# Kernel optimization log

Hardware: AMD Instinct MI355X
Metric: run time of the kernel (lower is better)

## Reference

```python
import jax, jax.numpy as jnp
import numpy as np

N_NODES = 50000


def gcn_conv(x, W, b, src, dst, n_nodes):
    """PyG GCNConv: h = x @ W; add self-loops; symmetric deg^-1/2 norm; scatter-sum; + bias."""
    h = x @ W  # [N, out]
    # degree including self-loop (edge weight 1)
    ones = jnp.ones(dst.shape[0], dtype=x.dtype)
    deg = jax.ops.segment_sum(ones, dst, num_segments=n_nodes) + 1.0  # [N]
    dinv = jax.lax.rsqrt(deg)  # deg >= 1 always (self-loop)
    # per-edge norm = dinv[src] * dinv[dst]; gather, scale, scatter-add
    msg = h[src] * (dinv[src] * dinv[dst])[:, None]  # [E, out]
    agg = jax.ops.segment_sum(msg, dst, num_segments=n_nodes)
    # self-loop contribution: norm_ii = dinv[i]^2
    agg = agg + h * (dinv * dinv)[:, None]
    return agg + b


def setup_inputs() -> dict:
    key = jax.random.key(0)
    k1, k2, k3, k4, k5 = jax.random.split(key, 5)
    in_dim, hidden_dim = 128, 128
    x = jax.random.normal(k1, (N_NODES, in_dim), dtype=jnp.float32)
    edge_index = jax.random.randint(k2, (2, 800000), 0, N_NODES, dtype=jnp.int64)
    W1 = jax.random.normal(k3, (in_dim, hidden_dim), dtype=jnp.float32) * 0.05
    b1 = jnp.zeros((hidden_dim,), dtype=jnp.float32)
    W2 = jax.random.normal(k4, (hidden_dim, 1), dtype=jnp.float32) * 0.05
    b2 = jnp.zeros((1,), dtype=jnp.float32)
    return {"x": x, "edge_index": edge_index, "W1": W1, "b1": b1, "W2": W2, "b2": b2}


def reference(x, edge_index, W1, b1, W2, b2):
    src, dst = edge_index[0], edge_index[1]
    n = x.shape[0]
    h = gcn_conv(x, W1, b1, src, dst, n)
    h = jax.nn.relu(h)  # dropout is identity in eval mode
    out = gcn_conv(h, W2, b2, src, dst, n)
    return out.squeeze(-1)  # [N]
```

## Files before the change

### kernel.cpp

```cpp
#include <hip/hip_runtime.h>
#include <hip/hip_fp16.h>

#define DIM 128
#define SCAN_TILE 2048
#define NCHK 256
#define BKT_SHIFT 8
#define BCAP 8192

typedef _Float16 half8v __attribute__((ext_vector_type(8)));
typedef float    floatx4 __attribute__((ext_vector_type(4)));

__device__ __forceinline__ void h8_to_f8(float4 raw, float* o) {
    half8v hh = __builtin_bit_cast(half8v, raw);
#pragma unroll
    for (int k = 0; k < 8; ++k) o[k] = (float)hh[k];
}
__device__ __forceinline__ void h8_fma_mix(float4 raw, float dv, float* a) {
    half8v hh = __builtin_bit_cast(half8v, raw);
#pragma unroll
    for (int k = 0; k < 8; ++k) a[k] = fmaf((float)hh[k], dv, a[k]);
}

__global__ __launch_bounds__(256) void init_kernel(const float* __restrict__ W,
                                                   _Float16* __restrict__ Wt,
                                                   int* __restrict__ tile_pub) {
    int i = blockIdx.x * 256 + threadIdx.x;
    if (i < 32) tile_pub[i] = 0;
    if (i < DIM * DIM) {
        int k = i >> 7, c = i & 127;
        Wt[(size_t)c * DIM + k] = (_Float16)W[i];
    }
}

__global__ __launch_bounds__(256) void k1gemm_kernel(const int* __restrict__ dst,
                                                     int E, int n, int nbkt,
                                                     unsigned short* __restrict__ rank_local,
                                                     int* __restrict__ blockhist,
                                                     const float* __restrict__ x,
                                                     const _Float16* __restrict__ Wt,
                                                     __half* __restrict__ hs) {
    const int tid = threadIdx.x;
    const int bid = blockIdx.x;
    const bool isK1 = ((bid & 3) == 0) && ((bid >> 2) < NCHK);
    if (isK1) {
        __shared__ int bhl[256];
        const int cid = bid >> 2;
        const int echk = (E + NCHK - 1) / NCHK;
        const int e0 = cid * echk, e1 = min(E, e0 + echk);
        bhl[tid] = 0;
        __syncthreads();
        for (int e = e0 + tid; e < e1; e += 256) {
            int d = min(max(dst[e], 0), n - 1);
            int r = atomicAdd(&bhl[d >> BKT_SHIFT], 1);
            rank_local[e] = (unsigned short)r;
        }
        __syncthreads();
        for (int b = tid; b < nbkt; b += 256)
            blockhist[b * NCHK + cid] = bhl[b];
        return;
    }
    const int g   = bid - 1 - min(bid >> 2, NCHK - 1);
    const int wv  = tid >> 6;
    const int l   = tid & 63;
    const int lr  = l & 15;
    const int lk  = l >> 4;
    const int brow = g * 64 + wv * 16;
    const int arow = min(brow + lr, n - 1);

    floatx4 acc[8];
#pragma unroll
    for (int ct = 0; ct < 8; ++ct) acc[ct] = (floatx4){0.f, 0.f, 0.f, 0.f};

#pragma unroll
    for (int kb = 0; kb < 4; ++kb) {
        const float* ap = x + (size_t)arow * DIM + kb * 32 + lk * 8;
        float4 a0 = ((const float4*)ap)[0];
        float4 a1 = ((const float4*)ap)[1];
        half8v af;
        af[0] = (_Float16)a0.x; af[1] = (_Float16)a0.y;
        af[2] = (_Float16)a0.z; af[3] = (_Float16)a0.w;
        af[4] = (_Float16)a1.x; af[5] = (_Float16)a1.y;
        af[6] = (_Float16)a1.z; af[7] = (_Float16)a1.w;
#pragma unroll
        for (int ct = 0; ct < 8; ++ct) {
            half8v bf = *(const half8v*)(Wt + (size_t)(ct * 16 + lr) * DIM + kb * 32 + lk * 8);
            acc[ct] = __builtin_amdgcn_mfma_f32_16x16x32_f16(af, bf, acc[ct], 0, 0, 0);
        }
    }
#pragma unroll
    for (int j = 0; j < 4; ++j) {
        int orow = brow + lk * 4 + j;
        if (orow < n) {
#pragma unroll
            for (int ct = 0; ct < 8; ++ct)
                hs[(size_t)orow * DIM + ct * 16 + lr] = __float2half(acc[ct][j]);
        }
    }
}

__global__ __launch_bounds__(256) void scan_kernel(const int* __restrict__ in,
                                                   int L, int* __restrict__ outp,
                                                   int* __restrict__ tile_pub) {
    __shared__ int s[256];
    __shared__ int bbase;
    const int t = threadIdx.x;
    const int b = blockIdx.x;
    const int base = b * SCAN_TILE + t * 8;
    int v[8];
    int tsum = 0;
#pragma unroll
    for (int k = 0; k < 8; ++k) {
        int i = base + k;
        v[k] = (i < L) ? in[i] : 0;
        tsum += v[k];
    }
    s[t] = tsum;
    if (t == 0) bbase = 0;
    __syncthreads();
#pragma unroll
    for (int off = 1; off < 256; off <<= 1) {
        int u = (t >= off) ? s[t - off] : 0;
        __syncthreads();
        s[t] += u;
        __syncthreads();
    }
    if (t == 255)
        __hip_atomic_store(&tile_pub[b], s[255] + 1, __ATOMIC_RELEASE, __HIP_MEMORY_SCOPE_AGENT);
    if (t < b) {
        int val;
        do {
            val = __hip_atomic_load(&tile_pub[t], __ATOMIC_ACQUIRE, __HIP_MEMORY_SCOPE_AGENT);
        } while (val == 0);
        atomicAdd(&bbase, val - 1);
    }
    __syncthreads();
    int run = bbase + s[t] - tsum;
#pragma unroll
    for (int k = 0; k < 8; ++k) {
        int i = base + k;
        if (i < L) outp[i] = run;
        run += v[k];
    }
}

__global__ __launch_bounds__(256) void scat_kernel(const int* __restrict__ src,
                                                   const int* __restrict__ dst,
                                                   const unsigned short* __restrict__ rank_local,
                                                   int E, int n,
                                                   const int* __restrict__ bhoff,
                                                   unsigned int* __restrict__ bedge) {
    const int cid = blockIdx.x;
    const int echk = (E + NCHK - 1) / NCHK;
    const int e0 = cid * echk, e1 = min(E, e0 + echk);
    for (int e = e0 + threadIdx.x; e < e1; e += 256) {
        int s = min(max(src[e], 0), n - 1);
        int d = min(max(dst[e], 0), n - 1);
        int bkt = d >> BKT_SHIFT;
        int pos = bhoff[bkt * NCHK + cid] + rank_local[e];
        bedge[pos] = (unsigned int)s | ((unsigned int)(d & 255) << 16);
    }
}

__global__ __launch_bounds__(256) void bcsr_kernel(const int* __restrict__ bhoff,
                                                   const unsigned int* __restrict__ bedge,
                                                   int E, int n, int nbkt,
                                                   unsigned short* __restrict__ csr,
                                                   int* __restrict__ row_off,
                                                   float* __restrict__ dinv) {
    __shared__ unsigned int ed[BCAP];
    __shared__ unsigned short rk[BCAP];
    __shared__ int h[256], s2[256], offx[256];
    const int t = threadIdx.x;
    const int g = blockIdx.x;
    const int beg = bhoff[g * NCHK];
    const int end = (g == nbkt - 1) ? E : bhoff[(g + 1) * NCHK];
    const int cntb = min(end - beg, BCAP);

    h[t] = 0;
    __syncthreads();
    for (int i = t; i < cntb; i += 256) {
        unsigned int u = bedge[beg + i];
        ed[i] = u;
        rk[i] = (unsigned short)atomicAdd(&h[(u >> 16) & 255], 1);
    }
    __syncthreads();
    int hv = h[t];
    s2[t] = hv;
    __syncthreads();
#pragma unroll
    for (int off = 1; off < 256; off <<= 1) {
        int u = (t >= off) ? s2[t - off] : 0;
        __syncthreads();
        s2[t] += u;
        __syncthreads();
    }
    offx[t] = s2[t] - hv;
    __syncthreads();
    int node = (g << BKT_SHIFT) + t;
    if (node < n) {
        row_off[node] = beg + offx[t];
        dinv[node] = rsqrtf((float)hv + 1.0f);
    }
    if (g == nbkt - 1 && t == 0) row_off[n] = E;
    for (int i = t; i < cntb; i += 256) {
        unsigned int u = ed[i];
        csr[beg + offx[(u >> 16) & 255] + rk[i]] = (unsigned short)(u & 0xFFFF);
    }
}

__global__ __launch_bounds__(256) void gather1_kernel(const int* __restrict__ row_off,
                                                      const unsigned short* __restrict__ csr,
                                                      const __half* __restrict__ hs,
                                                      const float* __restrict__ dinv,
                                                      const float* __restrict__ b1,
                                                      const float* __restrict__ W2,
                                                      float* __restrict__ ss, int n) {
    const int wave = threadIdx.x >> 6;
    const int lane = threadIdx.x & 63;
    const int node = blockIdx.x * 4 + wave;
    if (node >= n) return;

    const int rs = row_off[node];
    const int re = row_off[node + 1];
    const int q = lane & 7;
    const int g = lane >> 3;
    const float4* hs4 = (const float4*)hs;

    float a[16];
#pragma unroll
    for (int k = 0; k < 16; ++k) a[k] = 0.f;

    for (int j = rs + g; j < re; j += 8) {
        int s = csr[j];
        float dvs = dinv[s];
        const float4* rp = hs4 + (size_t)s * 16 + 2 * q;
        float4 r0 = rp[0];
        float4 r1 = rp[1];
        h8_fma_mix(r0, dvs, a);
        h8_fma_mix(r1, dvs, a + 8);
    }

#pragma unroll
    for (int k = 0; k < 16; ++k) {
        a[k] += __shfl_xor(a[k], 8, 64);
        a[k] += __shfl_xor(a[k], 16, 64);
        a[k] += __shfl_xor(a[k], 32, 64);
    }

    float dv = dinv[node];
    float hv[16];
    h8_to_f8(hs4[(size_t)node * 16 + 2 * q], hv);
    h8_to_f8(hs4[(size_t)node * 16 + 2 * q + 1], hv + 8);

    float bv[16], wv[16];
#pragma unroll
    for (int u = 0; u < 4; ++u) {
        float4 bq = ((const float4*)b1)[4 * q + u];
        float4 wq = ((const float4*)W2)[4 * q + u];
        bv[4 * u + 0] = bq.x; bv[4 * u + 1] = bq.y; bv[4 * u + 2] = bq.z; bv[4 * u + 3] = bq.w;
        wv[4 * u + 0] = wq.x; wv[4 * u + 1] = wq.y; wv[4 * u + 2] = wq.z; wv[4 * u + 3] = wq.w;
    }

    float p = 0.f;
#pragma unroll
    for (int k = 0; k < 16; ++k) {
        float h1 = fmaxf(fmaf(dv, fmaf(dv, hv[k], a[k]), bv[k]), 0.f);
        p = fmaf(h1, wv[k], p);
    }
    p += __shfl_xor(p, 1, 64);
    p += __shfl_xor(p, 2, 64);
    p += __shfl_xor(p, 4, 64);
    if (lane == 0) ss[node] = p * dv;
}

__global__ __launch_bounds__(256) void gather2_kernel(const int* __restrict__ row_off,
                                                      const unsigned short* __restrict__ csr,
                                                      const float* __restrict__ ss,
                                                      const float* __restrict__ dinv,
                                                      const float* __restrict__ b2,
                                                      float* __restrict__ out, int n) {
    int i = blockIdx.x * 256 + threadIdx.x;
    if (i >= n) return;
    int rs = row_off[i], re = row_off[i + 1];
    float s0 = 0.f, s1 = 0.f, s2 = 0.f, s3 = 0.f;
    int j = rs;
    for (; j + 3 < re; j += 4) {
        int c0 = csr[j], c1 = csr[j + 1], c2 = csr[j + 2], c3 = csr[j + 3];
        s0 += ss[c0]; s1 += ss[c1]; s2 += ss[c2]; s3 += ss[c3];
    }
    for (; j < re; ++j) s0 += ss[csr[j]];
    out[i] = fmaf(dinv[i], (s0 + s1) + (s2 + s3) + ss[i], b2[0]);
}

extern "C" void kernel_launch(void* const* d_in, const int* in_sizes, int n_in,
                              void* d_out, int out_size, void* d_ws, size_t ws_size,
                              hipStream_t stream) {
    const float* x   = (const float*)d_in[0];
    const int*   ei  = (const int*)d_in[1];
    const float* W1  = (const float*)d_in[2];
    const float* b1  = (const float*)d_in[3];
    const float* W2  = (const float*)d_in[4];
    const float* b2  = (const float*)d_in[5];
    float*       out = (float*)d_out;

    const int n = in_sizes[0] / DIM;
    const int E = in_sizes[1] / 2;
    const int* srcI = ei;
    const int* dstI = ei + E;
    const int nbkt = (n + 255) >> BKT_SHIFT;
    const int L = nbkt * NCHK;
    const int scan_tiles = (L + SCAN_TILE - 1) / SCAN_TILE;

    char* ws = (char*)d_ws;
    size_t off = 0;
    auto alloc = [&](size_t bytes) { void* p = ws + off; off = (off + bytes + 511) & ~(size_t)511; return p; };
    float*          dinv     = (float*)alloc((size_t)n * 4);
    int*            row_off  = (int*)  alloc((size_t)(n + 1) * 4);
    unsigned short* rank_loc = (unsigned short*)alloc((size_t)E * 2);
    int*            bhist    = (int*)  alloc((size_t)L * 4);
    int*            bhoff    = (int*)  alloc((size_t)L * 4);
    int*            tile_pub = (int*)  alloc((size_t)32 * 4);
    unsigned int*   bedge    = (unsigned int*)alloc((size_t)E * 4);
    unsigned short* csr      = (unsigned short*)alloc((size_t)E * 2);
    __half*         hs       = (__half*)alloc((size_t)n * DIM * 2);
    float*          ss       = (float*)alloc((size_t)n * 4);
    _Float16*       Wt       = (_Float16*)alloc((size_t)DIM * DIM * 2);

    const int gemm_blocks = (n + 63) / 64;

    init_kernel<<<64, 256, 0, stream>>>(W1, Wt, tile_pub);
    k1gemm_kernel<<<NCHK + gemm_blocks, 256, 0, stream>>>(dstI, E, n, nbkt, rank_loc,
                                                          bhist, x, Wt, hs);
    scan_kernel<<<scan_tiles, 256, 0, stream>>>(bhist, L, bhoff, tile_pub);
    scat_kernel<<<NCHK, 256, 0, stream>>>(srcI, dstI, rank_loc, E, n, bhoff, bedge);
    bcsr_kernel<<<nbkt, 256, 0, stream>>>(bhoff, bedge, E, n, nbkt, csr, row_off, dinv);
    gather1_kernel<<<(n + 3) / 4, 256, 0, stream>>>(row_off, csr, hs, dinv, b1, W2, ss, n);
    gather2_kernel<<<(n + 255) / 256, 256, 0, stream>>>(row_off, csr, ss, dinv, b2, out, n);
}
```

Measured before the change: 111.7 us.

## Stage CSR neighbor indices and dinv in LDS for 16-node gather1 blocks

gather1 now handles 16 nodes per block, with each wave processing 4 nodes in sequence. Before the gather, the block cooperatively loads the CSR index slice and the matching dinv values into shared memory, up to 512 edges. This takes the dependent csr-then-dinv global load chain out of the inner gather loop and leaves only the hs row loads there. The cost is two block barriers, shared memory use and less parallelism per node, since nodes inside a wave are now processed serially.

```diff
diff --git a/kernel.cpp b/kernel.cpp
--- a/kernel.cpp
+++ b/kernel.cpp
@@ -6,6 +6,8 @@
 #define NCHK 256
 #define BKT_SHIFT 8
 #define BCAP 8192
+#define G1NODES 16
+#define G1CAP 512
 
 typedef _Float16 half8v __attribute__((ext_vector_type(8)));
 typedef float    floatx4 __attribute__((ext_vector_type(4)));
@@ -215,62 +217,94 @@
                                                       const float* __restrict__ b1,
                                                       const float* __restrict__ W2,
                                                       float* __restrict__ ss, int n) {
-    const int wave = threadIdx.x >> 6;
-    const int lane = threadIdx.x & 63;
-    const int node = blockIdx.x * 4 + wave;
-    if (node >= n) return;
-
-    const int rs = row_off[node];
-    const int re = row_off[node + 1];
+    __shared__ unsigned short ecsr[G1CAP];
+    __shared__ float edinv[G1CAP];
+    __shared__ int roff[G1NODES + 1];
+
+    const int tid  = threadIdx.x;
+    const int node0 = blockIdx.x * G1NODES;
+    const int nlast = min(node0 + G1NODES, n);
+
+    if (tid <= G1NODES) {
+        int idx = min(node0 + tid, n);
+        roff[tid] = row_off[idx];
+    }
+    __syncthreads();
+    const int base = roff[0];
+    const int cnt  = roff[nlast - node0] - base;
+    const int staged = min(cnt, G1CAP);
+    for (int i = tid; i < staged; i += 256) {
+        int s = csr[base + i];
+        ecsr[i] = (unsigned short)s;
+        edinv[i] = dinv[s];
+    }
+    __syncthreads();
+
+    const int wave = tid >> 6;
+    const int lane = tid & 63;
     const int q = lane & 7;
     const int g = lane >> 3;
     const float4* hs4 = (const float4*)hs;
 
-    float a[16];
-#pragma unroll
-    for (int k = 0; k < 16; ++k) a[k] = 0.f;
-
-    for (int j = rs + g; j < re; j += 8) {
-        int s = csr[j];
-        float dvs = dinv[s];
-        const float4* rp = hs4 + (size_t)s * 16 + 2 * q;
-        float4 r0 = rp[0];
-        float4 r1 = rp[1];
-        h8_fma_mix(r0, dvs, a);
-        h8_fma_mix(r1, dvs, a + 8);
-    }
-
-#pragma unroll
-    for (int k = 0; k < 16; ++k) {
-        a[k] += __shfl_xor(a[k], 8, 64);
-        a[k] += __shfl_xor(a[k], 16, 64);
-        a[k] += __shfl_xor(a[k], 32, 64);
-    }
-
-    float dv = dinv[node];
-    float hv[16];
-    h8_to_f8(hs4[(size_t)node * 16 + 2 * q], hv);
-    h8_to_f8(hs4[(size_t)node * 16 + 2 * q + 1], hv + 8);
-
-    float bv[16], wv[16];
-#pragma unroll
-    for (int u = 0; u < 4; ++u) {
-        float4 bq = ((const float4*)b1)[4 * q + u];
-        float4 wq = ((const float4*)W2)[4 * q + u];
-        bv[4 * u + 0] = bq.x; bv[4 * u + 1] = bq.y; bv[4 * u + 2] = bq.z; bv[4 * u + 3] = bq.w;
-        wv[4 * u + 0] = wq.x; wv[4 * u + 1] = wq.y; wv[4 * u + 2] = wq.z; wv[4 * u + 3] = wq.w;
-    }
-
-    float p = 0.f;
-#pragma unroll
-    for (int k = 0; k < 16; ++k) {
-        float h1 = fmaxf(fmaf(dv, fmaf(dv, hv[k], a[k]), bv[k]), 0.f);
-        p = fmaf(h1, wv[k], p);
-    }
-    p += __shfl_xor(p, 1, 64);
-    p += __shfl_xor(p, 2, 64);
-    p += __shfl_xor(p, 4, 64);
-    if (lane == 0) ss[node] = p * dv;
+#pragma unroll 1
+    for (int i = 0; i < 4; ++i) {
+        const int node = node0 + wave * 4 + i;
+        if (node >= n) break;
+        const int rsL = roff[wave * 4 + i] - base;
+        const int reL = roff[wave * 4 + i + 1] - base;
+
+        float a[16];
+#pragma unroll
+        for (int k = 0; k < 16; ++k) a[k] = 0.f;
+
+        for (int j = rsL + g; j < reL; j += 8) {
+            int s; float dvs;
+            if (j < G1CAP) {
+                s = ecsr[j];
+                dvs = edinv[j];
+            } else {
+                s = csr[base + j];
+                dvs = dinv[s];
+            }
+            const float4* rp = hs4 + (size_t)s * 16 + 2 * q;
+            float4 r0 = rp[0];
+            float4 r1 = rp[1];
+            h8_fma_mix(r0, dvs, a);
+            h8_fma_mix(r1, dvs, a + 8);
+        }
+
+#pragma unroll
+        for (int k = 0; k < 16; ++k) {
+            a[k] += __shfl_xor(a[k], 8, 64);
+            a[k] += __shfl_xor(a[k], 16, 64);
+            a[k] += __shfl_xor(a[k], 32, 64);
+        }
+
+        float dv = dinv[node];
+        float hv[16];
+        h8_to_f8(hs4[(size_t)node * 16 + 2 * q], hv);
+        h8_to_f8(hs4[(size_t)node * 16 + 2 * q + 1], hv + 8);
+
+        float bv[16], wv[16];
+#pragma unroll
+        for (int u = 0; u < 4; ++u) {
+            float4 bq = ((const float4*)b1)[4 * q + u];
+            float4 wq = ((const float4*)W2)[4 * q + u];
+            bv[4 * u + 0] = bq.x; bv[4 * u + 1] = bq.y; bv[4 * u + 2] = bq.z; bv[4 * u + 3] = bq.w;
+            wv[4 * u + 0] = wq.x; wv[4 * u + 1] = wq.y; wv[4 * u + 2] = wq.z; wv[4 * u + 3] = wq.w;
+        }
+
+        float p = 0.f;
+#pragma unroll
+        for (int k = 0; k < 16; ++k) {
+            float h1 = fmaxf(fmaf(dv, fmaf(dv, hv[k], a[k]), bv[k]), 0.f);
+            p = fmaf(h1, wv[k], p);
+        }
+        p += __shfl_xor(p, 1, 64);
+        p += __shfl_xor(p, 2, 64);
+        p += __shfl_xor(p, 4, 64);
+        if (lane == 0) ss[node] = p * dv;
+    }
 }
 
 __global__ __launch_bounds__(256) void gather2_kernel(const int* __restrict__ row_off,
@@ -334,6 +368,7 @@
     scan_kernel<<<scan_tiles, 256, 0, stream>>>(bhist, L, bhoff, tile_pub);
     scat_kernel<<<NCHK, 256, 0, stream>>>(srcI, dstI, rank_loc, E, n, bhoff, bedge);
     bcsr_kernel<<<nbkt, 256, 0, stream>>>(bhoff, bedge, E, n, nbkt, csr, row_off, dinv);
-    gather1_kernel<<<(n + 3) / 4, 256, 0, stream>>>(row_off, csr, hs, dinv, b1, W2, ss, n);
+    gather1_kernel<<<(n + G1NODES - 1) / G1NODES, 256, 0, stream>>>(row_off, csr, hs, dinv,
+                                                                    b1, W2, ss, n);
     gather2_kernel<<<(n + 255) / 256, 256, 0, stream>>>(row_off, csr, ss, dinv, b2, out, n);
 }
```

After: 114.0 us. 2.1% more time.
